# Performance work log

Measured on AMD Instinct MI355X. Metric: run time of the kernel, lower is better.

The kernel has to match this reference:

```python
import jax, jax.numpy as jnp
import numpy as np

DIM = 2048
H = 16
D = 128          # head_dim
INNER = H * D    # == DIM
N_IMG = 257
EPS = 1e-6


def rms_norm(x, scale, eps=EPS):
    # flax nnx.RMSNorm over last axis: x * rsqrt(mean(x^2)+eps) * scale
    ms = jnp.mean(jnp.square(x), axis=-1, keepdims=True)
    return x * jax.lax.rsqrt(ms + eps) * scale


def sdpa(q, k, v):
    # q: (B,S,H,D), k/v: (B,L,H,D) -> (B,S,H,D); matches jax.nn.dot_product_attention
    scale = 1.0 / jnp.sqrt(jnp.asarray(D, q.dtype))
    scores = jnp.einsum('bshd,blhd->bhsl', q, k) * scale
    attn = jax.nn.softmax(scores, axis=-1)
    return jnp.einsum('bhsl,blhd->bshd', attn, v)


def setup_inputs() -> dict:
    key = jax.random.key(0)
    ks = jax.random.split(key, 16)
    std = 1.0 / np.sqrt(DIM)
    inp = {
        'x': jax.random.normal(ks[0], (2, 4096, DIM), jnp.float32),
        'context': jax.random.normal(ks[1], (2, 769, DIM), jnp.float32),
        'q_w': jax.random.normal(ks[2], (DIM, INNER), jnp.float32) * std,
        'q_b': jnp.zeros((INNER,), jnp.float32),
        'k_w': jax.random.normal(ks[3], (DIM, INNER), jnp.float32) * std,
        'k_b': jnp.zeros((INNER,), jnp.float32),
        'v_w': jax.random.normal(ks[4], (DIM, INNER), jnp.float32) * std,
        'v_b': jnp.zeros((INNER,), jnp.float32),
        'ki_w': jax.random.normal(ks[5], (DIM, INNER), jnp.float32) * std,
        'ki_b': jnp.zeros((INNER,), jnp.float32),
        'vi_w': jax.random.normal(ks[6], (DIM, INNER), jnp.float32) * std,
        'vi_b': jnp.zeros((INNER,), jnp.float32),
        'o_w': jax.random.normal(ks[7], (INNER, DIM), jnp.float32) * std,
        'o_b': jnp.zeros((DIM,), jnp.float32),
        'nq_s': jnp.ones((INNER,), jnp.float32),
        'nkt_s': jnp.ones((INNER,), jnp.float32),
        'nki_s': jnp.ones((INNER,), jnp.float32),
    }
    return inp


def reference(x, context, q_w, q_b, k_w, k_b, v_w, v_b, ki_w, ki_b, vi_w, vi_b,
              o_w, o_b, nq_s, nkt_s, nki_s):
    B, S, _ = x.shape
    img_ctx = context[:, :N_IMG]
    txt_ctx = context[:, N_IMG:]

    q = rms_norm(x @ q_w + q_b, nq_s).reshape(B, S, H, D)

    k_txt = rms_norm(txt_ctx @ k_w + k_b, nkt_s).reshape(B, -1, H, D)
    v_txt = (txt_ctx @ v_w + v_b).reshape(B, -1, H, D)
    out_txt = sdpa(q, k_txt, v_txt)

    k_img = rms_norm(img_ctx @ ki_w + ki_b, nki_s).reshape(B, -1, H, D)
    v_img = (img_ctx @ vi_w + vi_b).reshape(B, -1, H, D)
    out_img = sdpa(q, k_img, v_img)

    out = (out_txt + out_img).reshape(B, S, INNER)
    return out @ o_w + o_b
```

## Files before the change

### kernel.cpp

```cpp
#include <hip/hip_runtime.h>

typedef unsigned short u16;
typedef short s8v __attribute__((ext_vector_type(8)));
typedef float f32x4 __attribute__((ext_vector_type(4)));

#define MFMA16(a, b, c) __builtin_amdgcn_mfma_f32_16x16x32_bf16((a), (b), (c), 0, 0, 0)
#define GLDS16(gp, lp)                                                         \
  __builtin_amdgcn_global_load_lds(                                            \
      (const __attribute__((address_space(1))) void*)(gp),                     \
      (__attribute__((address_space(3))) void*)(lp), 16, 0, 0)

__device__ __forceinline__ float bf2f(u16 u) {
  unsigned int i = ((unsigned int)u) << 16;
  float f;
  __builtin_memcpy(&f, &i, 4);
  return f;
}
__device__ __forceinline__ u16 f2bf(float f) {
  unsigned int u;
  __builtin_memcpy(&u, &f, 4);
  unsigned int r = (u + 0x7FFFu + ((u >> 16) & 1u)) >> 16;
  return (u16)r;
}

__global__ __launch_bounds__(256) void cvt_f32_bf16(const float* __restrict__ s,
                                                    u16* __restrict__ d, long n) {
  long i = ((long)blockIdx.x * 256 + threadIdx.x) * 4;
  if (i + 3 < n) {
    float4 v = *(const float4*)(s + i);
    ushort4 o;
    o.x = f2bf(v.x); o.y = f2bf(v.y); o.z = f2bf(v.z); o.w = f2bf(v.w);
    *(ushort4*)(d + i) = o;
  }
}

struct TransposeBatch {
  const float* src[6];
  u16* dst[6];
};

__global__ __launch_bounds__(256) void transpose2048_batch(TransposeBatch p) {
  const float* __restrict__ W = p.src[blockIdx.z];
  u16* __restrict__ Wt = p.dst[blockIdx.z];
  __shared__ u16 t[64][65];
  int c0 = blockIdx.x * 64, r0 = blockIdx.y * 64;
  int x = threadIdx.x & 63, y = threadIdx.x >> 6;
  for (int yy = y; yy < 64; yy += 4)
    t[yy][x] = f2bf(W[(long)(r0 + yy) * 2048 + c0 + x]);
  __syncthreads();
  for (int yy = y; yy < 64; yy += 4)
    Wt[(long)(c0 + yy) * 2048 + r0 + x] = t[x][yy];
}

template <int OUTF, int DUAL>
__global__ __launch_bounds__(256, 2) void gemm_bias_bt(
    const u16* __restrict__ A, const u16* __restrict__ Bt,
    const float* __restrict__ bias, const float* __restrict__ bias2,
    void* __restrict__ Yv, void* __restrict__ Yv2, int M, int rpb, int bstride,
    int roff) {
  __shared__ u16 smA[128 * 32];
  __shared__ u16 smB[128 * 32];
  const int tid = threadIdx.x;
  const int wave = tid >> 6, lane = tid & 63;
  const int lo = lane & 15, qd = lane >> 4;
  const int m0 = blockIdx.x * 128, n0 = blockIdx.y * 128;
  const int wm = (wave & 1) * 64, wn = (wave >> 1) * 64;

  const u16* aG[2];
  const u16* bG[2];
  u16* aL[2];
  u16* bL[2];
#pragma unroll
  for (int r = 0; r < 2; ++r) {
    int c = (wave * 2 + r) * 64 + lane;
    int row = c >> 2, seg = c & 3;
    int gr = m0 + row;
    if (gr > M - 1) gr = M - 1;
    long grow = (long)(gr / rpb) * bstride + roff + (gr % rpb);
    aG[r] = A + grow * 2048 + seg * 8;
    bG[r] = Bt + (long)(n0 + row) * 2048 + seg * 8;
    aL[r] = smA + (wave * 2 + r) * 512;
    bL[r] = smB + (wave * 2 + r) * 512;
  }

  f32x4 acc[4][4] = {};
  for (int k0 = 0; k0 < 2048; k0 += 32) {
    GLDS16(aG[0] + k0, aL[0]);
    GLDS16(aG[1] + k0, aL[1]);
    GLDS16(bG[0] + k0, bL[0]);
    GLDS16(bG[1] + k0, bL[1]);
    __syncthreads();
    s8v af[4], bf[4];
#pragma unroll
    for (int i = 0; i < 4; i++)
      af[i] = *(const s8v*)(smA + (wm + i * 16 + lo) * 32 + qd * 8);
#pragma unroll
    for (int i = 0; i < 4; i++)
      bf[i] = *(const s8v*)(smB + (wn + i * 16 + lo) * 32 + qd * 8);
#pragma unroll
    for (int i = 0; i < 4; i++)
#pragma unroll
      for (int j = 0; j < 4; j++) acc[i][j] = MFMA16(af[i], bf[j], acc[i][j]);
    __syncthreads();
  }
#pragma unroll
  for (int j = 0; j < 4; j++) {
    int nf = n0 + wn + j * 16 + lo;
    const float* bp = bias;
    void* yp = Yv;
    int n = nf;
    if (DUAL && nf >= 2048) {
      bp = bias2;
      yp = Yv2;
      n = nf - 2048;
    }
    float bv = bp[n];
#pragma unroll
    for (int i = 0; i < 4; i++) {
      int mb = m0 + wm + i * 16 + qd * 4;
#pragma unroll
      for (int r = 0; r < 4; r++) {
        int m = mb + r;
        if (m < M) {
          float val = acc[i][j][r] + bv;
          if (OUTF)
            ((float*)yp)[(long)m * 2048 + n] = val;
          else
            ((u16*)yp)[(long)m * 2048 + n] = f2bf(val);
        }
      }
    }
  }
}

template <int OUTF>
__global__ __launch_bounds__(512, 2) void gemm256(
    const u16* __restrict__ A, const u16* __restrict__ Bt,
    const float* __restrict__ bias, void* __restrict__ Yv) {
  __shared__ u16 smA[2][16384];
  __shared__ u16 smB[2][16384];
  const int tid = threadIdx.x;
  const int wave = tid >> 6, lane = tid & 63;
  const int lo = lane & 15, qd = lane >> 4;
  const int m0 = blockIdx.x * 256, n0 = blockIdx.y * 256;
  const int wm = (wave >> 2) * 128, wn = (wave & 3) * 64;
  const int wbase = (tid & ~63);

  auto stage_h = [&](int b, int t, int half) {
#pragma unroll
    for (int j = half * 2; j < half * 2 + 2; ++j) {
      int ci = j * 512 + tid;
      int r = ci >> 3, c = ci & 7;
      GLDS16(A + (long)(m0 + r) * 2048 + t * 64 + ((c ^ (r & 7)) << 3),
             &smA[b][(j * 512 + wbase) * 8]);
    }
#pragma unroll
    for (int j = half * 2; j < half * 2 + 2; ++j) {
      int ci = j * 512 + tid;
      int r = ci >> 3, c = ci & 7;
      GLDS16(Bt + (long)(n0 + r) * 2048 + t * 64 + ((c ^ (r & 7)) << 3),
             &smB[b][(j * 512 + wbase) * 8]);
    }
  };
  auto rdA = [&](int b, int ks, int mf) {
    int r = wm + mf * 16 + lo;
    int sc = (ks * 4 + qd) ^ (r & 7);
    return *(const s8v*)(&smA[b][r * 64 + sc * 8]);
  };
  auto rdB = [&](int b, int ks, int nf) {
    int r = wn + nf * 16 + lo;
    int sc = (ks * 4 + qd) ^ (r & 7);
    return *(const s8v*)(&smB[b][r * 64 + sc * 8]);
  };

  f32x4 acc[8][4] = {};
  stage_h(0, 0, 0); stage_h(0, 0, 1);
  stage_h(1, 1, 0); stage_h(1, 1, 1);
  asm volatile("s_waitcnt vmcnt(8)" ::: "memory");
  __builtin_amdgcn_s_barrier();

  for (int t = 0; t < 32; ++t) {
    const int b = t & 1;
    s8v af[8], bf[4];
#pragma unroll
    for (int mf = 0; mf < 8; ++mf) af[mf] = rdA(b, 0, mf);
#pragma unroll
    for (int nf = 0; nf < 4; ++nf) bf[nf] = rdB(b, 0, nf);
    if (t < 31) stage_h(b ^ 1, t + 1, 0);
    __builtin_amdgcn_s_setprio(1);
#pragma unroll
    for (int mf = 0; mf < 8; ++mf)
#pragma unroll
      for (int nf = 0; nf < 4; ++nf)
        acc[mf][nf] = MFMA16(af[mf], bf[nf], acc[mf][nf]);
    __builtin_amdgcn_s_setprio(0);
    __builtin_amdgcn_s_barrier();
#pragma unroll
    for (int mf = 0; mf < 8; ++mf) af[mf] = rdA(b, 1, mf);
#pragma unroll
    for (int nf = 0; nf < 4; ++nf) bf[nf] = rdB(b, 1, nf);
    if (t < 31) stage_h(b ^ 1, t + 1, 1);
    __builtin_amdgcn_s_setprio(1);
#pragma unroll
    for (int mf = 0; mf < 8; ++mf)
#pragma unroll
      for (int nf = 0; nf < 4; ++nf)
        acc[mf][nf] = MFMA16(af[mf], bf[nf], acc[mf][nf]);
    __builtin_amdgcn_s_setprio(0);
    asm volatile("s_waitcnt vmcnt(0)" ::: "memory");
    __builtin_amdgcn_s_barrier();
  }

#pragma unroll
  for (int nf = 0; nf < 4; ++nf) {
    int n = n0 + wn + nf * 16 + lo;
    float bv = bias[n];
#pragma unroll
    for (int mf = 0; mf < 8; ++mf) {
      int mb = m0 + wm + mf * 16 + qd * 4;
#pragma unroll
      for (int r = 0; r < 4; ++r) {
        float val = acc[mf][nf][r] + bv;
        if (OUTF)
          ((float*)Yv)[(long)(mb + r) * 2048 + n] = val;
        else
          ((u16*)Yv)[(long)(mb + r) * 2048 + n] = f2bf(val);
      }
    }
  }
}

__global__ __launch_bounds__(256) void rmsnorm_rows(u16* __restrict__ X,
                                                    const float* __restrict__ sc) {
  long row = blockIdx.x;
  u16* xr = X + row * 2048;
  int tid = threadIdx.x;
  s8v v = *(const s8v*)(xr + tid * 8);
  float f[8], ss = 0.f;
#pragma unroll
  for (int j = 0; j < 8; j++) {
    f[j] = bf2f((u16)v[j]);
    ss += f[j] * f[j];
  }
  for (int o = 1; o < 64; o <<= 1) ss += __shfl_xor(ss, o);
  __shared__ float wsum[4];
  if ((tid & 63) == 0) wsum[tid >> 6] = ss;
  __syncthreads();
  float tot = wsum[0] + wsum[1] + wsum[2] + wsum[3];
  float rs = rsqrtf(tot * (1.f / 2048.f) + 1e-6f);
  float4 s0 = *(const float4*)(sc + tid * 8);
  float4 s1 = *(const float4*)(sc + tid * 8 + 4);
  float scv[8] = {s0.x, s0.y, s0.z, s0.w, s1.x, s1.y, s1.z, s1.w};
  s8v o8;
#pragma unroll
  for (int j = 0; j < 8; j++) o8[j] = (short)f2bf(f[j] * rs * scv[j]);
  *(s8v*)(xr + tid * 8) = o8;
}

__global__ __launch_bounds__(256) void repack_vt(const u16* __restrict__ V,
                                                 u16* __restrict__ VT, int L,
                                                 int Lpad) {
  int bh = blockIdx.z;
  int b = bh >> 4, h = bh & 15;
  int l0 = blockIdx.x * 64, d0 = blockIdx.y * 64;
  __shared__ u16 t[64][65];
  int x = threadIdx.x & 63, y = threadIdx.x >> 6;
  for (int yy = y; yy < 64; yy += 4) {
    int l = l0 + yy;
    u16 val = 0;
    if (l < L) val = V[((long)(b * L + l)) * 2048 + h * 128 + d0 + x];
    t[yy][x] = val;
  }
  __syncthreads();
  for (int yy = y; yy < 64; yy += 4) {
    int d = d0 + yy;
    int l = l0 + x;
    if (l < Lpad) VT[((long)bh * 128 + d) * Lpad + l] = t[x][yy];
  }
}

template <int LT, int LPT, int NTT, int LI, int LPI, int NTI>
__global__ __launch_bounds__(256, 2) void cross_attn_fused(
    const u16* __restrict__ Q, const u16* __restrict__ Kt,
    const u16* __restrict__ VTt, const u16* __restrict__ Ki,
    const u16* __restrict__ VTi, u16* __restrict__ O) {
  const int tid = threadIdx.x, wave = tid >> 6, lane = tid & 63;
  const int lo = lane & 15, qd = lane >> 4;
  const int id = blockIdx.x;
  const int xp = id & 7, xr = id >> 3;
  const int t = xr & 31;
  const int f = xp * 4 + (xr >> 5);
  const int h = f & 15, b = f >> 4;
  const int q0 = t * 128 + wave * 32;

  __shared__ u16 smem[38912];
  u16* lk = smem;
  u16* lv = smem + 8192;
  u16* pls = smem + 16384;
  u16* oTs = smem + 21504;

  const u16* Kbt = Kt + ((long)b * LT) * 2048 + h * 128;
  const u16* VTbt = VTt + ((long)(b * 16 + h)) * 128 * LPT;
  const u16* Kbi = Ki + ((long)b * LI) * 2048 + h * 128;
  const u16* VTbi = VTi + ((long)(b * 16 + h)) * 128 * LPI;

  auto stage = [&](int pb, int gt) {
    const u16* Kb;
    const u16* VTb;
    int kt, L, LPAD;
    if (gt < NTT) {
      Kb = Kbt; VTb = VTbt; kt = gt; L = LT; LPAD = LPT;
    } else {
      Kb = Kbi; VTb = VTbi; kt = gt - NTT; L = LI; LPAD = LPI;
    }
#pragma unroll
    for (int j = 0; j < 2; ++j) {
      int ci = (wave * 2 + j) * 64 + lane;
      int r = ci >> 4, c = ci & 15;
      int key = kt * 32 + r;
      if (key > L - 1) key = L - 1;
      const u16* src = Kb + (long)key * 2048 + (c ^ (r & 7)) * 8;
      GLDS16(src, &lk[pb * 4096 + (wave * 2 + j) * 512]);
    }
#pragma unroll
    for (int j = 0; j < 2; ++j) {
      int ci = (wave * 2 + j) * 64 + lane;
      int d = ci >> 2, c = ci & 3;
      const u16* src = VTb + (long)d * LPAD + kt * 32 + (c ^ ((d >> 1) & 3)) * 8;
      GLDS16(src, &lv[pb * 4096 + (wave * 2 + j) * 512]);
    }
  };

  s8v aq[2][4];
#pragma unroll
  for (int qf = 0; qf < 2; ++qf) {
    const u16* qp =
        Q + ((long)(b * 4096 + q0 + qf * 16 + lo)) * 2048 + h * 128 + qd * 8;
#pragma unroll
    for (int ds = 0; ds < 4; ++ds) aq[qf][ds] = *(const s8v*)(qp + ds * 32);
  }

  const float SC = 0.08838834764831845f;
  const int vsw = (lo >> 1) & 3;

  auto tile_step = [&](int pb, int ktile, int Lcur, f32x4 (&oacc)[2][8],
                       float (&lsum)[2][4]) {
    s8v bk[2][4];
#pragma unroll
    for (int nf = 0; nf < 2; ++nf) {
      int r = nf * 16 + lo;
#pragma unroll
      for (int ds = 0; ds < 4; ++ds) {
        int cp = (ds * 4 + qd) ^ (r & 7);
        bk[nf][ds] = *(const s8v*)(&lk[pb * 4096 + r * 128 + cp * 8]);
      }
    }
    f32x4 sacc[2][2] = {};
    __builtin_amdgcn_s_setprio(1);
#pragma unroll
    for (int qf = 0; qf < 2; ++qf)
#pragma unroll
      for (int nf = 0; nf < 2; ++nf)
#pragma unroll
        for (int ds = 0; ds < 4; ++ds)
          sacc[qf][nf] = MFMA16(aq[qf][ds], bk[nf][ds], sacc[qf][nf]);
    __builtin_amdgcn_s_setprio(0);
    u16* pw = pls + wave * 1280;
#pragma unroll
    for (int qf = 0; qf < 2; ++qf)
#pragma unroll
      for (int nf = 0; nf < 2; ++nf) {
        int key = ktile * 32 + nf * 16 + lo;
        bool msk = key >= Lcur;
#pragma unroll
        for (int r = 0; r < 4; ++r) {
          float s = fminf(fmaf(sacc[qf][nf][r], SC, -12.f), 50.f);
          float p = msk ? 0.f : __expf(s);
          lsum[qf][r] += p;
          pw[(qf * 16 + qd * 4 + r) * 40 + nf * 16 + lo] = f2bf(p);
        }
      }
    s8v pa[2];
#pragma unroll
    for (int qf = 0; qf < 2; ++qf)
      pa[qf] = *(const s8v*)(pw + (qf * 16 + lo) * 40 + qd * 8);
    __builtin_amdgcn_s_setprio(1);
#pragma unroll
    for (int df = 0; df < 8; ++df) {
      int d = df * 16 + lo;
      s8v bv = *(const s8v*)(&lv[pb * 4096 + d * 32 + (qd ^ vsw) * 8]);
      oacc[0][df] = MFMA16(pa[0], bv, oacc[0][df]);
      oacc[1][df] = MFMA16(pa[1], bv, oacc[1][df]);
    }
    __builtin_amdgcn_s_setprio(0);
  };

  stage(0, 0);
  __syncthreads();

  u16* ep = oTs + wave * 4352;

  {
    f32x4 oT[2][8] = {};
    float lsT[2][4] = {};
#pragma unroll 2
    for (int kt = 0; kt < NTT; ++kt) {
      const int pb = kt & 1;
      stage(pb ^ 1, kt + 1);
      tile_step(pb, kt, LT, oT, lsT);
      __syncthreads();
    }
#pragma unroll
    for (int qf = 0; qf < 2; ++qf)
#pragma unroll
      for (int r = 0; r < 4; ++r) {
        float a = lsT[qf][r];
        for (int o = 1; o < 16; o <<= 1) a += __shfl_xor(a, o);
        lsT[qf][r] = 1.f / a;
      }
#pragma unroll
    for (int qf = 0; qf < 2; ++qf)
#pragma unroll
      for (int df = 0; df < 8; ++df)
#pragma unroll
        for (int r = 0; r < 4; ++r)
          ep[(qf * 16 + qd * 4 + r) * 136 + df * 16 + lo] =
              f2bf(oT[qf][df][r] * lsT[qf][r]);
  }

  f32x4 oI[2][8] = {};
  float lsI[2][4] = {};
#pragma unroll 2
  for (int kt = 0; kt < NTI; ++kt) {
    const int pb = kt & 1;
    if (kt + 1 < NTI) stage(pb ^ 1, NTT + kt + 1);
    tile_step(pb, kt, LI, oI, lsI);
    if (kt + 1 < NTI) __syncthreads();
  }

#pragma unroll
  for (int qf = 0; qf < 2; ++qf)
#pragma unroll
    for (int r = 0; r < 4; ++r) {
      float c = lsI[qf][r];
      for (int o = 1; o < 16; o <<= 1) c += __shfl_xor(c, o);
      lsI[qf][r] = 1.f / c;
    }
#pragma unroll
  for (int qf = 0; qf < 2; ++qf)
#pragma unroll
    for (int df = 0; df < 8; ++df)
#pragma unroll
      for (int r = 0; r < 4; ++r) {
        int idx = (qf * 16 + qd * 4 + r) * 136 + df * 16 + lo;
        float val = bf2f(ep[idx]) + oI[qf][df][r] * lsI[qf][r];
        ep[idx] = f2bf(val);
      }
  const int row = lane >> 1, half = lane & 1;
  const u16* srcp = ep + row * 136 + half * 64;
  u16* gdst = O + ((long)(b * 4096 + q0 + row)) * 2048 + h * 128 + half * 64;
#pragma unroll
  for (int c = 0; c < 8; ++c) *(s8v*)(gdst + c * 8) = *(const s8v*)(srcp + c * 8);
}

extern "C" void kernel_launch(void* const* d_in, const int* in_sizes, int n_in,
                              void* d_out, int out_size, void* d_ws,
                              size_t ws_size, hipStream_t stream) {
  const float* x = (const float*)d_in[0];
  const float* ctx = (const float*)d_in[1];
  const float* q_w = (const float*)d_in[2];
  const float* q_b = (const float*)d_in[3];
  const float* k_w = (const float*)d_in[4];
  const float* k_b = (const float*)d_in[5];
  const float* v_w = (const float*)d_in[6];
  const float* v_b = (const float*)d_in[7];
  const float* ki_w = (const float*)d_in[8];
  const float* ki_b = (const float*)d_in[9];
  const float* vi_w = (const float*)d_in[10];
  const float* vi_b = (const float*)d_in[11];
  const float* o_w = (const float*)d_in[12];
  const float* o_b = (const float*)d_in[13];
  const float* nq_s = (const float*)d_in[14];
  const float* nkt_s = (const float*)d_in[15];
  const float* nki_s = (const float*)d_in[16];
  float* out = (float*)d_out;
  u16* ws = (u16*)d_ws;

  u16* w0 = ws;
  u16* w1 = ws + 4194304L;
  u16* q = ws + 8388608L;
  u16* attn = ws + 25165824L;
  u16* xb = attn;
  u16* vtxt = attn;
  u16* vimg = attn + 2097152L;
  u16* ktxt = ws + 41943040L;
  u16* kimg = ws + 44040192L;
  u16* vttxt = ws + 45092864L;
  u16* vtimg = ws + 47190016L;
  u16* ctxb = ws + 48369664L;

  dim3 tb(256);

  cvt_f32_bf16<<<3076, tb, 0, stream>>>(ctx, ctxb, 3149824L);
  TransposeBatch tp;
  tp.src[0] = q_w;  tp.dst[0] = w0;
  tp.src[1] = o_w;  tp.dst[1] = w1;
  tp.src[2] = k_w;  tp.dst[2] = q;
  tp.src[3] = v_w;  tp.dst[3] = q + 4194304L;
  tp.src[4] = ki_w; tp.dst[4] = q + 8388608L;
  tp.src[5] = vi_w; tp.dst[5] = q + 12582912L;
  transpose2048_batch<<<dim3(32, 32, 6), tb, 0, stream>>>(tp);

  gemm_bias_bt<0, 1><<<dim3(8, 32), tb, 0, stream>>>(
      ctxb, q, k_b, v_b, ktxt, vtxt, 1024, 512, 769, 257);
  gemm_bias_bt<0, 1><<<dim3(5, 32), tb, 0, stream>>>(
      ctxb, q + 8388608L, ki_b, vi_b, kimg, vimg, 514, 257, 769, 0);

  rmsnorm_rows<<<1024, tb, 0, stream>>>(ktxt, nkt_s);
  rmsnorm_rows<<<514, tb, 0, stream>>>(kimg, nki_s);
  repack_vt<<<dim3(8, 2, 32), tb, 0, stream>>>(vtxt, vttxt, 512, 512);
  repack_vt<<<dim3(5, 2, 32), tb, 0, stream>>>(vimg, vtimg, 257, 288);

  cvt_f32_bf16<<<16384, tb, 0, stream>>>(x, xb, 16777216L);
  gemm256<0><<<dim3(32, 8), dim3(512), 0, stream>>>(xb, w0, q_b, q);
  rmsnorm_rows<<<8192, tb, 0, stream>>>(q, nq_s);

  cross_attn_fused<512, 512, 16, 257, 288, 9><<<1024, tb, 0, stream>>>(
      q, ktxt, vttxt, kimg, vtimg, attn);

  gemm256<1><<<dim3(32, 8), dim3(512), 0, stream>>>(attn, w1, o_b, out);
}
```

Before: 575.5 us.

## Compute softmax row sums via MFMA with ones vector and skip masking on full tiles

The softmax denominator is now produced by an extra MFMA that multiplies the bf16 probability tile by a vector of ones. This replaces the per-element scalar accumulation and the cross-lane shuffle reduction. Masking is compiled out for all key tiles except the last image tile. In the projection GEMM, both halves of the next tile are prefetched before the first half's MFMAs rather than split across the two halves. The sum now uses bf16-rounded probabilities, and dropping the text-tile masking assumes the text length fills whole tiles.

```diff
diff --git a/kernel.cpp b/kernel.cpp
--- a/kernel.cpp
+++ b/kernel.cpp
@@ -22,6 +22,11 @@
   unsigned int r = (u + 0x7FFFu + ((u >> 16) & 1u)) >> 16;
   return (u16)r;
 }
+
+template <bool B>
+struct MaskTag {
+  static constexpr bool do_mask = B;
+};
 
 __global__ __launch_bounds__(256) void cvt_f32_bf16(const float* __restrict__ s,
                                                     u16* __restrict__ d, long n) {
@@ -186,7 +191,10 @@
     for (int mf = 0; mf < 8; ++mf) af[mf] = rdA(b, 0, mf);
 #pragma unroll
     for (int nf = 0; nf < 4; ++nf) bf[nf] = rdB(b, 0, nf);
-    if (t < 31) stage_h(b ^ 1, t + 1, 0);
+    if (t < 31) {
+      stage_h(b ^ 1, t + 1, 0);
+      stage_h(b ^ 1, t + 1, 1);
+    }
     __builtin_amdgcn_s_setprio(1);
 #pragma unroll
     for (int mf = 0; mf < 8; ++mf)
@@ -199,7 +207,6 @@
     for (int mf = 0; mf < 8; ++mf) af[mf] = rdA(b, 1, mf);
 #pragma unroll
     for (int nf = 0; nf < 4; ++nf) bf[nf] = rdB(b, 1, nf);
-    if (t < 31) stage_h(b ^ 1, t + 1, 1);
     __builtin_amdgcn_s_setprio(1);
 #pragma unroll
     for (int mf = 0; mf < 8; ++mf)
@@ -342,9 +349,13 @@
 
   const float SC = 0.08838834764831845f;
   const int vsw = (lo >> 1) & 3;
+  s8v vones;
+#pragma unroll
+  for (int j = 0; j < 8; ++j) vones[j] = (short)0x3F80;
 
   auto tile_step = [&](int pb, int ktile, int Lcur, f32x4 (&oacc)[2][8],
-                       float (&lsum)[2][4]) {
+                       f32x4 (&lones)[2], auto mt) {
+    constexpr bool DOMASK = decltype(mt)::do_mask;
     s8v bk[2][4];
 #pragma unroll
     for (int nf = 0; nf < 2; ++nf) {
@@ -370,13 +381,16 @@
     for (int qf = 0; qf < 2; ++qf)
 #pragma unroll
       for (int nf = 0; nf < 2; ++nf) {
-        int key = ktile * 32 + nf * 16 + lo;
-        bool msk = key >= Lcur;
+        bool msk = false;
+        if constexpr (DOMASK) {
+          int key = ktile * 32 + nf * 16 + lo;
+          msk = key >= Lcur;
+        }
 #pragma unroll
         for (int r = 0; r < 4; ++r) {
           float s = fminf(fmaf(sacc[qf][nf][r], SC, -12.f), 50.f);
-          float p = msk ? 0.f : __expf(s);
-          lsum[qf][r] += p;
+          float p = __expf(s);
+          if constexpr (DOMASK) p = msk ? 0.f : p;
           pw[(qf * 16 + qd * 4 + r) * 40 + nf * 16 + lo] = f2bf(p);
         }
       }
@@ -392,6 +406,8 @@
       oacc[0][df] = MFMA16(pa[0], bv, oacc[0][df]);
       oacc[1][df] = MFMA16(pa[1], bv, oacc[1][df]);
     }
+    lones[0] = MFMA16(pa[0], vones, lones[0]);
+    lones[1] = MFMA16(pa[1], vones, lones[1]);
     __builtin_amdgcn_s_setprio(0);
   };
 
@@ -402,22 +418,19 @@
 
   {
     f32x4 oT[2][8] = {};
-    float lsT[2][4] = {};
+    f32x4 lonesT[2] = {};
 #pragma unroll 2
     for (int kt = 0; kt < NTT; ++kt) {
       const int pb = kt & 1;
       stage(pb ^ 1, kt + 1);
-      tile_step(pb, kt, LT, oT, lsT);
+      tile_step(pb, kt, LT, oT, lonesT, MaskTag<false>{});
       __syncthreads();
     }
+    float invT[2][4];
 #pragma unroll
     for (int qf = 0; qf < 2; ++qf)
 #pragma unroll
-      for (int r = 0; r < 4; ++r) {
-        float a = lsT[qf][r];
-        for (int o = 1; o < 16; o <<= 1) a += __shfl_xor(a, o);
-        lsT[qf][r] = 1.f / a;
-      }
+      for (int r = 0; r < 4; ++r) invT[qf][r] = 1.f / lonesT[qf][r];
 #pragma unroll
     for (int qf = 0; qf < 2; ++qf)
 #pragma unroll
@@ -425,27 +438,25 @@
 #pragma unroll
         for (int r = 0; r < 4; ++r)
           ep[(qf * 16 + qd * 4 + r) * 136 + df * 16 + lo] =
-              f2bf(oT[qf][df][r] * lsT[qf][r]);
+              f2bf(oT[qf][df][r] * invT[qf][r]);
   }
 
   f32x4 oI[2][8] = {};
-  float lsI[2][4] = {};
+  f32x4 lonesI[2] = {};
 #pragma unroll 2
-  for (int kt = 0; kt < NTI; ++kt) {
+  for (int kt = 0; kt < NTI - 1; ++kt) {
     const int pb = kt & 1;
-    if (kt + 1 < NTI) stage(pb ^ 1, NTT + kt + 1);
-    tile_step(pb, kt, LI, oI, lsI);
-    if (kt + 1 < NTI) __syncthreads();
-  }
-
+    stage(pb ^ 1, NTT + kt + 1);
+    tile_step(pb, kt, LI, oI, lonesI, MaskTag<false>{});
+    __syncthreads();
+  }
+  tile_step((NTI - 1) & 1, NTI - 1, LI, oI, lonesI, MaskTag<true>{});
+
+  float invI[2][4];
 #pragma unroll
   for (int qf = 0; qf < 2; ++qf)
 #pragma unroll
-    for (int r = 0; r < 4; ++r) {
-      float c = lsI[qf][r];
-      for (int o = 1; o < 16; o <<= 1) c += __shfl_xor(c, o);
-      lsI[qf][r] = 1.f / c;
-    }
+    for (int r = 0; r < 4; ++r) invI[qf][r] = 1.f / lonesI[qf][r];
 #pragma unroll
   for (int qf = 0; qf < 2; ++qf)
 #pragma unroll
@@ -453,7 +464,7 @@
 #pragma unroll
       for (int r = 0; r < 4; ++r) {
         int idx = (qf * 16 + qd * 4 + r) * 136 + df * 16 + lo;
-        float val = bf2f(ep[idx]) + oI[qf][df][r] * lsI[qf][r];
+        float val = bf2f(ep[idx]) + oI[qf][df][r] * invI[qf][r];
         ep[idx] = f2bf(val);
       }
   const int row = lane >> 1, half = lane & 1;
```

New measurement: 566.2 us. Within noise of the previous version (-1.6%).
